# Kernel optimization log

Hardware: AMD Instinct MI355X
Metric: run time of the kernel (lower is better)

The kernel has to match this reference:

```python
import jax, jax.numpy as jnp
import numpy as np

THRESH = 0.5

def setup_inputs() -> dict:
    key = jax.random.key(0)
    mask = jax.random.uniform(key, (128, 1, 512, 512), dtype=jnp.float32)
    return {"mask": mask}

def _minmax_plus1(hit, full):
    # hit: [N, L] bool. Returns (min_idx, max_idx+1); (0, full) if no hit in row.
    any_hit = jnp.any(hit, axis=1)
    lo = jnp.argmax(hit, axis=1).astype(jnp.int32)
    hi = (hit.shape[1] - jnp.argmax(hit[:, ::-1], axis=1)).astype(jnp.int32)  # last hit + 1
    lo = jnp.where(any_hit, lo, jnp.int32(0))
    hi = jnp.where(any_hit, hi, jnp.int32(full))
    return lo, hi

def reference(mask):
    # mask: [N, 1, H, W] -> bbox [N, 4] = (y_min, x_min, y_max, x_max)
    m = jnp.squeeze(mask, axis=1)            # [N, H, W]
    N, H, W = m.shape
    wmat = jnp.max(m, axis=1) >= THRESH      # [N, W] column hits
    hmat = jnp.max(m, axis=2) >= THRESH      # [N, H] row hits
    xmin, xmax = _minmax_plus1(wmat, W)
    ymin, ymax = _minmax_plus1(hmat, H)
    return jnp.stack((ymin, xmin, ymax, xmax), axis=-1)  # [N, 4] int32
```

## Files before the change

kernel.cpp:

```cpp
#include <hip/hip_runtime.h>
#include <climits>


#define THRESH 0.5f

static constexpr int N = 128;
static constexpr int H = 512;
static constexpr int W = 512;
static constexpr int G = 32;
static constexpr int ROWS = H / G;
static constexpr int BLK = 256;
static constexpr int W4 = W / 4;
static constexpr int ITER = ROWS * W4 / BLK;

typedef float f32x4 __attribute__((ext_vector_type(4)));

__global__ __launch_bounds__(BLK)
void bbox_partial(const float* __restrict__ mask, int* __restrict__ partials) {
    const int n = blockIdx.x;
    const int g = blockIdx.y;
    const f32x4* base =
        (const f32x4*)(mask + (size_t)n * H * W + (size_t)g * ROWS * W);

    const int c  = threadIdx.x & (W4 - 1);
    const int rb = threadIdx.x >> 7;

    f32x4 v[ITER];
    #pragma unroll
    for (int k = 0; k < ITER; ++k)
        v[k] = __builtin_nontemporal_load(&base[threadIdx.x + k * BLK]);

    int ymin = INT_MAX, ymax = -1;
    float m0 = 0.f, m1 = 0.f, m2 = 0.f, m3 = 0.f;

    #pragma unroll
    for (int k = 0; k < ITER; ++k) {
        float mx = fmaxf(fmaxf(v[k].x, v[k].y), fmaxf(v[k].z, v[k].w));
        int r = 2 * k + rb;
        if (mx >= THRESH) { ymin = min(ymin, r); ymax = max(ymax, r); }
        m0 = fmaxf(m0, v[k].x); m1 = fmaxf(m1, v[k].y);
        m2 = fmaxf(m2, v[k].z); m3 = fmaxf(m3, v[k].w);
    }

    if (ymax >= 0) { ymin += g * ROWS; ymax += g * ROWS; }

    const int w = c << 2;
    int xmin = INT_MAX, xmax = -1;
    if (m0 >= THRESH) { xmin = w;                xmax = w;                }
    if (m1 >= THRESH) { xmin = min(xmin, w + 1); xmax = max(xmax, w + 1); }
    if (m2 >= THRESH) { xmin = min(xmin, w + 2); xmax = max(xmax, w + 2); }
    if (m3 >= THRESH) { xmin = min(xmin, w + 3); xmax = max(xmax, w + 3); }

    #pragma unroll
    for (int off = 32; off > 0; off >>= 1) {
        ymin = min(ymin, __shfl_down(ymin, off, 64));
        ymax = max(ymax, __shfl_down(ymax, off, 64));
        xmin = min(xmin, __shfl_down(xmin, off, 64));
        xmax = max(xmax, __shfl_down(xmax, off, 64));
    }

    __shared__ int s[BLK / 64][4];
    const int wave = threadIdx.x >> 6;
    const int lane = threadIdx.x & 63;
    if (lane == 0) {
        s[wave][0] = ymin; s[wave][1] = ymax; s[wave][2] = xmin; s[wave][3] = xmax;
    }
    __syncthreads();
    if (threadIdx.x == 0) {
        int a = s[0][0], b = s[0][1], cc = s[0][2], d = s[0][3];
        #pragma unroll
        for (int wv = 1; wv < BLK / 64; ++wv) {
            a  = min(a,  s[wv][0]); b = max(b, s[wv][1]);
            cc = min(cc, s[wv][2]); d = max(d, s[wv][3]);
        }
        ((int4*)partials)[n * G + g] = make_int4(a, b, cc, d);
    }
}

__global__ __launch_bounds__(128)
void bbox_final(const int* __restrict__ partials, int* __restrict__ out) {
    const int n = threadIdx.x;
    if (n >= N) return;
    int ymin = INT_MAX, ymax = -1, xmin = INT_MAX, xmax = -1;
    const int4* p = (const int4*)partials + n * G;
    #pragma unroll
    for (int g = 0; g < G; ++g) {
        int4 q = p[g];
        ymin = min(ymin, q.x); ymax = max(ymax, q.y);
        xmin = min(xmin, q.z); xmax = max(xmax, q.w);
    }
    int4 r;
    if (ymax < 0) r = make_int4(0, 0, H, W);
    else          r = make_int4(ymin, xmin, ymax + 1, xmax + 1);
    ((int4*)out)[n] = r;
}

extern "C" void kernel_launch(void* const* d_in, const int* in_sizes, int n_in,
                              void* d_out, int out_size, void* d_ws, size_t ws_size,
                              hipStream_t stream) {
    const float* mask = (const float*)d_in[0];
    int* partials = (int*)d_ws;
    int* out = (int*)d_out;

    dim3 grid(N, G);
    bbox_partial<<<grid, BLK, 0, stream>>>(mask, partials);
    bbox_final<<<1, 128, 0, stream>>>(partials, out);
}
```

Baseline: 177.3 us.

## Early-exit when border rows and columns all hit, fuse into one kernel

Each image first checks its first and last row and first and last column against the threshold. If all four borders contain a hit, the bounding box must be the full image, so the block writes that result and skips scanning the image. Otherwise a single 1024-thread block per image scans the whole image and writes the final box directly, which removes the partials buffer and the second kernel launch. The result is exact for any input, but the speedup depends on border hits being common; when the check fails there are only 128 blocks, which may underuse the GPU.

```diff
diff --git a/kernel.cpp b/kernel.cpp
--- a/kernel.cpp
+++ b/kernel.cpp
@@ -7,42 +7,49 @@
 static constexpr int N = 128;
 static constexpr int H = 512;
 static constexpr int W = 512;
-static constexpr int G = 32;
-static constexpr int ROWS = H / G;
-static constexpr int BLK = 256;
+static constexpr int BLK = 1024;
 static constexpr int W4 = W / 4;
-static constexpr int ITER = ROWS * W4 / BLK;
+static constexpr int ITER = (H * W4) / BLK;
 
 typedef float f32x4 __attribute__((ext_vector_type(4)));
 
 __global__ __launch_bounds__(BLK)
-void bbox_partial(const float* __restrict__ mask, int* __restrict__ partials) {
+void bbox_kernel(const float* __restrict__ mask, int* __restrict__ out) {
     const int n = blockIdx.x;
-    const int g = blockIdx.y;
-    const f32x4* base =
-        (const f32x4*)(mask + (size_t)n * H * W + (size_t)g * ROWS * W);
+    const int t = threadIdx.x;
+    const float* img = mask + (size_t)n * H * W;
 
-    const int c  = threadIdx.x & (W4 - 1);
-    const int rb = threadIdx.x >> 7;
+    __shared__ int sflag[4];
+    if (t < 4) sflag[t] = 0;
+    __syncthreads();
 
-    f32x4 v[ITER];
-    #pragma unroll
-    for (int k = 0; k < ITER; ++k)
-        v[k] = __builtin_nontemporal_load(&base[threadIdx.x + k * BLK]);
+    const int half = t >> 9;
+    const int i    = t & 511;
+    const float rv = img[(size_t)(half ? (H - 1) : 0) * W + i];
+    const float cv = img[(size_t)i * W + (half ? (W - 1) : 0)];
+    if (rv >= THRESH) sflag[half]     = 1;
+    if (cv >= THRESH) sflag[2 + half] = 1;
+    __syncthreads();
 
+    if (sflag[0] & sflag[1] & sflag[2] & sflag[3]) {
+        if (t == 0) ((int4*)out)[n] = make_int4(0, 0, H, W);
+        return;
+    }
+
+    const int c = t & (W4 - 1);
     int ymin = INT_MAX, ymax = -1;
     float m0 = 0.f, m1 = 0.f, m2 = 0.f, m3 = 0.f;
+    const f32x4* b4 = (const f32x4*)img;
 
-    #pragma unroll
+    #pragma unroll 8
     for (int k = 0; k < ITER; ++k) {
-        float mx = fmaxf(fmaxf(v[k].x, v[k].y), fmaxf(v[k].z, v[k].w));
-        int r = 2 * k + rb;
+        f32x4 v = __builtin_nontemporal_load(&b4[t + k * BLK]);
+        float mx = fmaxf(fmaxf(v.x, v.y), fmaxf(v.z, v.w));
+        int r = (t >> 7) + (k << 3);
         if (mx >= THRESH) { ymin = min(ymin, r); ymax = max(ymax, r); }
-        m0 = fmaxf(m0, v[k].x); m1 = fmaxf(m1, v[k].y);
-        m2 = fmaxf(m2, v[k].z); m3 = fmaxf(m3, v[k].w);
+        m0 = fmaxf(m0, v.x); m1 = fmaxf(m1, v.y);
+        m2 = fmaxf(m2, v.z); m3 = fmaxf(m3, v.w);
     }
-
-    if (ymax >= 0) { ymin += g * ROWS; ymax += g * ROWS; }
 
     const int w = c << 2;
     int xmin = INT_MAX, xmax = -1;
@@ -60,49 +67,30 @@
     }
 
     __shared__ int s[BLK / 64][4];
-    const int wave = threadIdx.x >> 6;
-    const int lane = threadIdx.x & 63;
+    const int wave = t >> 6;
+    const int lane = t & 63;
     if (lane == 0) {
         s[wave][0] = ymin; s[wave][1] = ymax; s[wave][2] = xmin; s[wave][3] = xmax;
     }
     __syncthreads();
-    if (threadIdx.x == 0) {
+    if (t == 0) {
         int a = s[0][0], b = s[0][1], cc = s[0][2], d = s[0][3];
         #pragma unroll
         for (int wv = 1; wv < BLK / 64; ++wv) {
             a  = min(a,  s[wv][0]); b = max(b, s[wv][1]);
             cc = min(cc, s[wv][2]); d = max(d, s[wv][3]);
         }
-        ((int4*)partials)[n * G + g] = make_int4(a, b, cc, d);
+        int4 r;
+        if (b < 0) r = make_int4(0, 0, H, W);
+        else       r = make_int4(a, cc, b + 1, d + 1);
+        ((int4*)out)[n] = r;
     }
-}
-
-__global__ __launch_bounds__(128)
-void bbox_final(const int* __restrict__ partials, int* __restrict__ out) {
-    const int n = threadIdx.x;
-    if (n >= N) return;
-    int ymin = INT_MAX, ymax = -1, xmin = INT_MAX, xmax = -1;
-    const int4* p = (const int4*)partials + n * G;
-    #pragma unroll
-    for (int g = 0; g < G; ++g) {
-        int4 q = p[g];
-        ymin = min(ymin, q.x); ymax = max(ymax, q.y);
-        xmin = min(xmin, q.z); xmax = max(xmax, q.w);
-    }
-    int4 r;
-    if (ymax < 0) r = make_int4(0, 0, H, W);
-    else          r = make_int4(ymin, xmin, ymax + 1, xmax + 1);
-    ((int4*)out)[n] = r;
 }
 
 extern "C" void kernel_launch(void* const* d_in, const int* in_sizes, int n_in,
                               void* d_out, int out_size, void* d_ws, size_t ws_size,
                               hipStream_t stream) {
     const float* mask = (const float*)d_in[0];
-    int* partials = (int*)d_ws;
     int* out = (int*)d_out;
-
-    dim3 grid(N, G);
-    bbox_partial<<<grid, BLK, 0, stream>>>(mask, partials);
-    bbox_final<<<1, 128, 0, stream>>>(partials, out);
+    bbox_kernel<<<dim3(N), BLK, 0, stream>>>(mask, out);
 }
```

New measurement: 162.4 us. 8.4% less time.
